# Kernel tuning notes

Measured on AMD Instinct MI355X. Metric: run time of the kernel, lower is better.

Reference implementation:

```python
import jax, jax.numpy as jnp
import numpy as np

D = 1024      # d_model
H = 16        # n_heads
HD = 64       # headdim
DFF = 2048    # per-expert ffn dim
E = 8         # n_experts
TOPK = 2
EPS = 1e-6
B, S = 2, 2048


def setup_inputs() -> dict:
    key = jax.random.key(0)
    ks = jax.random.split(key, 12)
    g = lambda i, shape, sc: (jax.random.normal(ks[i], shape, jnp.float32) * sc)
    return dict(
        x=g(0, (B, S, D), 1.0),
        pad_mask=jnp.ones((B, S), dtype=bool),
        norm1_w=jnp.ones((D,), jnp.float32),
        norm2_w=jnp.ones((D,), jnp.float32),
        Wr=g(1, (D, H * HD), 0.02),
        Wk=g(2, (D, H * HD), 0.02),
        Wv=g(3, (D, H * HD), 0.02),
        Wo=g(4, (H * HD, D), 0.02),
        decay=g(5, (H, HD), 0.5),   # time-decay param (w = exp(-exp(decay)))
        bonus=g(6, (H, HD), 0.5),   # RWKV 'u' first-token bonus
        router_w=g(7, (D, E), 0.02),
        w1=g(8, (E, D, DFF), 0.02),
        w2=g(9, (E, DFF, D), 0.02),
    )


def _rmsnorm(x, w):
    var = jnp.mean(x * x, axis=-1, keepdims=True)
    return x * jax.lax.rsqrt(var + EPS) * w


def _scan_dir(r, k, v, w, u):
    # r,k,v: [S,B,H,HD] ; w,u: [H,HD] ; RWKV-style linear-attention scan
    def step(St, rkv):
        r_t, k_t, v_t = rkv
        kv = jnp.einsum('bhk,bhv->bhkv', k_t, v_t)          # outer product
        y = jnp.einsum('bhk,bhkv->bhv', r_t, St + u[None, :, :, None] * kv)
        St = w[None, :, :, None] * St + kv                   # decayed state
        return St, y
    S0 = jnp.zeros((r.shape[1], H, HD, HD), r.dtype)
    _, ys = jax.lax.scan(step, S0, (r, k, v))
    return ys  # [S,B,H,HD]


def _bi_rwkv(x, pad_mask, Wr, Wk, Wv, Wo, decay, bonus):
    b, s, _ = x.shape
    r = (x @ Wr).reshape(b, s, H, HD)
    k = (x @ Wk).reshape(b, s, H, HD)
    v = (x @ Wv).reshape(b, s, H, HD)
    m = pad_mask[:, :, None, None].astype(x.dtype)
    k = k * m
    v = v * m
    w = jnp.exp(-jnp.exp(decay))  # decay in (0,1)
    rt = jnp.transpose(r, (1, 0, 2, 3))
    kt = jnp.transpose(k, (1, 0, 2, 3))
    vt = jnp.transpose(v, (1, 0, 2, 3))
    y_f = _scan_dir(rt, kt, vt, w, bonus)
    y_b = _scan_dir(rt[::-1], kt[::-1], vt[::-1], w, bonus)[::-1]
    y = jnp.transpose(y_f + y_b, (1, 0, 2, 3)).reshape(b, s, H * HD)
    return y @ Wo


def _moe_ffn(x, router_w, w1, w2):
    b, s, d = x.shape
    xt = x.reshape(-1, d)                                  # [T,D]
    T = xt.shape[0]
    probs = jax.nn.softmax(xt @ router_w, axis=-1)         # [T,E]
    topv, topi = jax.lax.top_k(probs, TOPK)
    gates = topv / jnp.sum(topv, axis=-1, keepdims=True)   # renormalized top-k
    gate_full = jnp.zeros((T, E), x.dtype).at[jnp.arange(T)[:, None], topi].set(gates)
    h = jax.nn.silu(jnp.einsum('td,edf->tef', xt, w1))     # all-expert dense ref
    out = jnp.einsum('tef,efd,te->td', h, w2, gate_full)
    # load-balancing aux loss
    frac = jnp.mean(jax.nn.one_hot(topi, E, dtype=x.dtype), axis=(0, 1))
    pmean = jnp.mean(probs, axis=0)
    aux = E * jnp.sum(frac * pmean)
    return out.reshape(b, s, d), aux


def reference(x, pad_mask, norm1_w, norm2_w, Wr, Wk, Wv, Wo, decay, bonus, router_w, w1, w2):
    # pre-norm RWKV block (dropout is identity at eval)
    x = x + _bi_rwkv(_rmsnorm(x, norm1_w), pad_mask, Wr, Wk, Wv, Wo, decay, bonus)
    ffn_out, aux = _moe_ffn(_rmsnorm(x, norm2_w), router_w, w1, w2)
    x = x + ffn_out
    return x, aux
```

## Files before the change

kernel.cpp:

```cpp
#include <hip/hip_runtime.h>

#define T_TOK 4096
#define DM 1024
#define NH 16
#define HDIM 64
#define DFF_ 2048
#define NE 8

typedef __bf16 bf16;
typedef __bf16 bf16x8 __attribute__((ext_vector_type(8)));
typedef __bf16 bf16x4 __attribute__((ext_vector_type(4)));
typedef float f32x4 __attribute__((ext_vector_type(4)));

__device__ __forceinline__ void gload_lds16(const bf16* g, bf16* l) {
  __builtin_amdgcn_global_load_lds(
      (const __attribute__((address_space(1))) void*)g,
      (__attribute__((address_space(3))) void*)l, 16, 0, 0);
}

template <int SPLIT>
__global__ __launch_bounds__(256) void rmsnorm_k(
    const float* __restrict__ x, const float* __restrict__ w,
    bf16* __restrict__ outh, bf16* __restrict__ outl) {
  const int t = blockIdx.x, tid = threadIdx.x;
  __shared__ float red[4];
  const f32x4 xv = *(const f32x4*)(x + (size_t)t * DM + tid * 4);
  float ss = xv.x * xv.x + xv.y * xv.y + xv.z * xv.z + xv.w * xv.w;
#pragma unroll
  for (int o = 32; o; o >>= 1) ss += __shfl_xor(ss, o);
  if ((tid & 63) == 0) red[tid >> 6] = ss;
  __syncthreads();
  const float rs = rsqrtf((red[0] + red[1] + red[2] + red[3]) * (1.f / DM) + 1e-6f);
  const f32x4 wv = *(const f32x4*)(w + tid * 4);
  float vv[4] = {xv.x * rs * wv.x, xv.y * rs * wv.y, xv.z * rs * wv.z, xv.w * rs * wv.w};
  bf16x4 h, l;
#pragma unroll
  for (int i = 0; i < 4; i++) {
    h[i] = (bf16)vv[i];
    l[i] = (bf16)(vv[i] - (float)h[i]);
  }
  *(bf16x4*)(outh + (size_t)t * DM + tid * 4) = h;
  if constexpr (SPLIT) *(bf16x4*)(outl + (size_t)t * DM + tid * 4) = l;
}

template <int SPLIT>
__global__ __launch_bounds__(256) void transpose_k(
    const float* __restrict__ src, bf16* __restrict__ dsth, bf16* __restrict__ dstl,
    int R, int C, long sstride, long dstride) {
  src += (long)blockIdx.z * sstride;
  dsth += (long)blockIdx.z * dstride;
  __shared__ float tle[32][33];
  const int tx = threadIdx.x, ty = threadIdx.y;
  const int c0 = blockIdx.x * 32, r0 = blockIdx.y * 32;
#pragma unroll
  for (int j = 0; j < 4; j++)
    tle[ty + 8 * j][tx] = src[(size_t)(r0 + ty + 8 * j) * C + c0 + tx];
  __syncthreads();
#pragma unroll
  for (int j = 0; j < 4; j++) {
    const float v = tle[tx][ty + 8 * j];
    const bf16 h = (bf16)v;
    dsth[(size_t)(c0 + ty + 8 * j) * R + r0 + tx] = h;
    if constexpr (SPLIT) {
      dstl[(size_t)(c0 + ty + 8 * j) * R + r0 + tx] = (bf16)(v - (float)h);
    }
  }
}

template <int K, int N, int MODE>
__global__ __launch_bounds__(256) void gemm_split_k(
    const bf16* __restrict__ Ah, const bf16* __restrict__ Al,
    const bf16* __restrict__ Bh, const bf16* __restrict__ Bl,
    float* __restrict__ Cout, const float* __restrict__ extraF,
    const int* __restrict__ pad) {
  __shared__ bf16 Ash[128 * 32], Asl[128 * 32], Bsh[128 * 32], Bsl[128 * 32];
  const int tid = threadIdx.x, w = tid >> 6, lane = tid & 63;
  const int n0 = blockIdx.x * 128, m0 = blockIdx.y * 128;
  const int sr0 = (w * 2 + 0) * 16 + (lane >> 2);
  const int sr1 = (w * 2 + 1) * 16 + (lane >> 2);
  const int sc = (lane & 3) * 8;
  const size_t ao0 = (size_t)(m0 + sr0) * K + sc, ao1 = (size_t)(m0 + sr1) * K + sc;
  const size_t bo0 = (size_t)(n0 + sr0) * K + sc, bo1 = (size_t)(n0 + sr1) * K + sc;

  f32x4 acc[4][4] = {};
  const int wm = w >> 1, wn = w & 1;
  const int fm = (wm * 64 + (lane & 15)) * 32 + (lane >> 4) * 8;
  const int fn = (wn * 64 + (lane & 15)) * 32 + (lane >> 4) * 8;
  const int l0 = (w * 2 + 0) * 512, l1 = (w * 2 + 1) * 512;

  for (int kt = 0; kt < K; kt += 32) {
    gload_lds16(Ah + ao0 + kt, Ash + l0);
    gload_lds16(Ah + ao1 + kt, Ash + l1);
    gload_lds16(Al + ao0 + kt, Asl + l0);
    gload_lds16(Al + ao1 + kt, Asl + l1);
    gload_lds16(Bh + bo0 + kt, Bsh + l0);
    gload_lds16(Bh + bo1 + kt, Bsh + l1);
    gload_lds16(Bl + bo0 + kt, Bsl + l0);
    gload_lds16(Bl + bo1 + kt, Bsl + l1);
    __syncthreads();
    bf16x8 afh[4], afl[4], bfh[4], bfl[4];
#pragma unroll
    for (int i = 0; i < 4; i++) {
      afh[i] = *(const bf16x8*)(Ash + fm + i * 512);
      afl[i] = *(const bf16x8*)(Asl + fm + i * 512);
      bfh[i] = *(const bf16x8*)(Bsh + fn + i * 512);
      bfl[i] = *(const bf16x8*)(Bsl + fn + i * 512);
    }
#pragma unroll
    for (int mi = 0; mi < 4; mi++)
#pragma unroll
      for (int ni = 0; ni < 4; ni++) {
        acc[mi][ni] = __builtin_amdgcn_mfma_f32_16x16x32_bf16(afh[mi], bfh[ni], acc[mi][ni], 0, 0, 0);
        acc[mi][ni] = __builtin_amdgcn_mfma_f32_16x16x32_bf16(afh[mi], bfl[ni], acc[mi][ni], 0, 0, 0);
        acc[mi][ni] = __builtin_amdgcn_mfma_f32_16x16x32_bf16(afl[mi], bfh[ni], acc[mi][ni], 0, 0, 0);
      }
    __syncthreads();
  }

  const int qr = (lane >> 4) * 4, cl = lane & 15;
#pragma unroll
  for (int mi = 0; mi < 4; mi++) {
#pragma unroll
    for (int r = 0; r < 4; r++) {
      const int row = m0 + wm * 64 + mi * 16 + qr + r;
      if constexpr (MODE == 0) {
        const float mf = (pad[row] != 0) ? 1.f : 0.f;
#pragma unroll
        for (int ni = 0; ni < 4; ni++) {
          const int col = n0 + wn * 64 + ni * 16 + cl;
          float v = acc[mi][ni][r];
          if (col >= DM) v *= mf;
          Cout[(size_t)row * N + col] = v;
        }
      } else {
#pragma unroll
        for (int ni = 0; ni < 4; ni++) {
          const int col = n0 + wn * 64 + ni * 16 + cl;
          Cout[(size_t)row * N + col] = acc[mi][ni][r] + extraF[(size_t)row * N + col];
        }
      }
    }
  }
}

template <int K, int MODE, int N>
__global__ __launch_bounds__(256) void gemm_k(
    const bf16* __restrict__ A, const bf16* __restrict__ BT, void* __restrict__ Cout,
    const float* __restrict__ extraF, const int* __restrict__ offsets,
    const int* __restrict__ counts, const int* __restrict__ ptoken) {
  __shared__ bf16 As[128 * 32];
  __shared__ bf16 Bs[128 * 32];
  const int tid = threadIdx.x, w = tid >> 6, lane = tid & 63;
  const int n0 = blockIdx.x * 128, m0 = blockIdx.y * 128;
  const int e = blockIdx.z;
  const int cnt = counts[e], offs = offsets[e];
  if (m0 >= cnt) return;
  const int sr0 = (w * 2 + 0) * 16 + (lane >> 2);
  const int sr1 = (w * 2 + 1) * 16 + (lane >> 2);
  const int sc = (lane & 3) * 8;
  const bf16 *a0, *a1;
  if constexpr (MODE == 2) {
    const int g0 = (m0 + sr0 < cnt) ? ptoken[offs + m0 + sr0] : 0;
    const int g1 = (m0 + sr1 < cnt) ? ptoken[offs + m0 + sr1] : 0;
    a0 = A + (size_t)g0 * K + sc;
    a1 = A + (size_t)g1 * K + sc;
  } else {
    const int g0 = offs + ((m0 + sr0 < cnt) ? m0 + sr0 : cnt - 1);
    const int g1 = offs + ((m0 + sr1 < cnt) ? m0 + sr1 : cnt - 1);
    a0 = A + (size_t)g0 * K + sc;
    a1 = A + (size_t)g1 * K + sc;
  }
  const bf16* btb = BT + (size_t)e * N * K;
  const bf16* b0 = btb + (size_t)(n0 + sr0) * K + sc;
  const bf16* b1 = btb + (size_t)(n0 + sr1) * K + sc;

  f32x4 acc[4][4] = {};
  const int wm = w >> 1, wn = w & 1;
  const int fm = (wm * 64 + (lane & 15)) * 32 + (lane >> 4) * 8;
  const int fn = (wn * 64 + (lane & 15)) * 32 + (lane >> 4) * 8;
  const int l0 = (w * 2 + 0) * 512, l1 = (w * 2 + 1) * 512;

  for (int kt = 0; kt < K; kt += 32) {
    gload_lds16(a0 + kt, As + l0);
    gload_lds16(a1 + kt, As + l1);
    gload_lds16(b0 + kt, Bs + l0);
    gload_lds16(b1 + kt, Bs + l1);
    __syncthreads();
    bf16x8 af[4], bfv[4];
#pragma unroll
    for (int i = 0; i < 4; i++) af[i] = *(const bf16x8*)(As + fm + i * 512);
#pragma unroll
    for (int i = 0; i < 4; i++) bfv[i] = *(const bf16x8*)(Bs + fn + i * 512);
#pragma unroll
    for (int mi = 0; mi < 4; mi++)
#pragma unroll
      for (int ni = 0; ni < 4; ni++)
        acc[mi][ni] =
            __builtin_amdgcn_mfma_f32_16x16x32_bf16(af[mi], bfv[ni], acc[mi][ni], 0, 0, 0);
    __syncthreads();
  }

  const int qr = (lane >> 4) * 4, cl = lane & 15;
#pragma unroll
  for (int mi = 0; mi < 4; mi++) {
#pragma unroll
    for (int r = 0; r < 4; r++) {
      const int row = m0 + wm * 64 + mi * 16 + qr + r;
      if (row >= cnt) continue;
      const size_t p = (size_t)(offs + row);
      if constexpr (MODE == 2) {
#pragma unroll
        for (int ni = 0; ni < 4; ni++) {
          const int col = n0 + wn * 64 + ni * 16 + cl;
          const float v = acc[mi][ni][r];
          ((bf16*)Cout)[p * N + col] = (bf16)(v / (1.f + __expf(-v)));
        }
      } else {
        const float g = extraF[p];
#pragma unroll
        for (int ni = 0; ni < 4; ni++) {
          const int col = n0 + wn * 64 + ni * 16 + cl;
          ((float*)Cout)[p * N + col] = acc[mi][ni][r] * g;
        }
      }
    }
  }
}

__global__ __launch_bounds__(256) void scan_k(
    const float* __restrict__ rkv, const float* __restrict__ decay,
    float* __restrict__ yacc) {
  const int wg = blockIdx.x;
  const int dir = wg & 1, kg = (wg >> 1) & 3, h = (wg >> 3) & 15, b = wg >> 7;
  const int tid = threadIdx.x, w = tid >> 6, lane = tid & 63;
  const int kb = kg * 16 + w * 4;
  __shared__ float ylds[4][16][64];

  const f32x4 dc = *(const f32x4*)(decay + h * HDIM + kb);
  const float wd0 = expf(-expf(dc.x)), wd1 = expf(-expf(dc.y));
  const float wd2 = expf(-expf(dc.z)), wd3 = expf(-expf(dc.w));

  const long base = (long)b * 2048 * 3072;
  const long start = dir ? (long)2047 * 3072 : 0;
  const long stp = dir ? -3072 : 3072;
  const float* rp = rkv + base + start + h * HDIM + kb;
  const float* kp = rp + 1024;
  const float* vp = rkv + base + start + 2048 + h * HDIM + lane;

  float S0 = 0.f, S1 = 0.f, S2 = 0.f, S3 = 0.f;
  f32x4 ka[8], ra[8], kc[8], rc[8];
  float va[8], vc[8], yb[16];
#pragma unroll
  for (int s = 0; s < 8; s++) {
    ka[s] = *(const f32x4*)(kp + (long)s * stp);
    ra[s] = *(const f32x4*)(rp + (long)s * stp);
    va[s] = vp[(long)s * stp];
  }
  for (int c = 0; c < 128; ++c) {
#pragma unroll
    for (int s = 0; s < 8; s++) {
      kc[s] = *(const f32x4*)(kp + (long)(8 + s) * stp);
      rc[s] = *(const f32x4*)(rp + (long)(8 + s) * stp);
      vc[s] = vp[(long)(8 + s) * stp];
    }
#pragma unroll
    for (int s = 0; s < 8; s++) {
      const float vv = va[s];
      const f32x4 Kv = ka[s], Rv = ra[s];
      yb[s] = Rv.x * S0 + Rv.y * S1 + Rv.z * S2 + Rv.w * S3;
      S0 = wd0 * S0 + Kv.x * vv;
      S1 = wd1 * S1 + Kv.y * vv;
      S2 = wd2 * S2 + Kv.z * vv;
      S3 = wd3 * S3 + Kv.w * vv;
    }
    if (c < 127) {
#pragma unroll
      for (int s = 0; s < 8; s++) {
        ka[s] = *(const f32x4*)(kp + (long)(16 + s) * stp);
        ra[s] = *(const f32x4*)(rp + (long)(16 + s) * stp);
        va[s] = vp[(long)(16 + s) * stp];
      }
    }
#pragma unroll
    for (int s = 0; s < 8; s++) {
      const float vv = vc[s];
      const f32x4 Kv = kc[s], Rv = rc[s];
      yb[8 + s] = Rv.x * S0 + Rv.y * S1 + Rv.z * S2 + Rv.w * S3;
      S0 = wd0 * S0 + Kv.x * vv;
      S1 = wd1 * S1 + Kv.y * vv;
      S2 = wd2 * S2 + Kv.z * vv;
      S3 = wd3 * S3 + Kv.w * vv;
    }
    kp += 16 * stp;
    rp += 16 * stp;
    vp += 16 * stp;
#pragma unroll
    for (int s = 0; s < 16; s++) ylds[w][s][lane] = yb[s];
    __syncthreads();
    {
      const int idx = tid * 4, tl = idx >> 6, v0 = idx & 63;
      const f32x4 s0 = *(const f32x4*)&ylds[0][tl][v0];
      const f32x4 s1 = *(const f32x4*)&ylds[1][tl][v0];
      const f32x4 s2 = *(const f32x4*)&ylds[2][tl][v0];
      const f32x4 s3 = *(const f32x4*)&ylds[3][tl][v0];
      const f32x4 sm = s0 + s1 + s2 + s3;
      const int sg = dir ? (2047 - (c * 16 + tl)) : (c * 16 + tl);
      float* yp = yacc + (size_t)(b * 2048 + sg) * DM + h * HDIM + v0;
      atomicAdd(yp + 0, sm.x);
      atomicAdd(yp + 1, sm.y);
      atomicAdd(yp + 2, sm.z);
      atomicAdd(yp + 3, sm.w);
    }
    __syncthreads();
  }
}

__global__ __launch_bounds__(256) void sum_k(
    const float* __restrict__ rkv, const float* __restrict__ bonus,
    const float* __restrict__ yacc, bf16* __restrict__ yh, bf16* __restrict__ yl) {
  const int tok = blockIdx.x, tid = threadIdx.x;
  const int hv = tid * 4;
  const float* bse = rkv + (size_t)tok * 3072;
  const f32x4 r4 = *(const f32x4*)(bse + hv);
  const f32x4 k4 = *(const f32x4*)(bse + 1024 + hv);
  const f32x4 v4 = *(const f32x4*)(bse + 2048 + hv);
  const f32x4 u4 = *(const f32x4*)(bonus + hv);
  float p = r4.x * u4.x * k4.x + r4.y * u4.y * k4.y + r4.z * u4.z * k4.z + r4.w * u4.w * k4.w;
  p += __shfl_xor(p, 1);
  p += __shfl_xor(p, 2);
  p += __shfl_xor(p, 4);
  p += __shfl_xor(p, 8);
  const float c2 = 2.f * p;
  const f32x4 ya = *(const f32x4*)(yacc + (size_t)tok * DM + hv);
  float yv[4] = {ya.x + c2 * v4.x, ya.y + c2 * v4.y, ya.z + c2 * v4.z, ya.w + c2 * v4.w};
  bf16x4 h, l;
#pragma unroll
  for (int i = 0; i < 4; i++) {
    h[i] = (bf16)yv[i];
    l[i] = (bf16)(yv[i] - (float)h[i]);
  }
  *(bf16x4*)(yh + (size_t)tok * DM + hv) = h;
  *(bf16x4*)(yl + (size_t)tok * DM + hv) = l;
}

__global__ __launch_bounds__(256) void router_k(
    const float* __restrict__ x2, const float* __restrict__ nw, const float* __restrict__ rw,
    float* __restrict__ gates, int* __restrict__ topi, float* __restrict__ prbuf) {
  const int t = blockIdx.x, tid = threadIdx.x, lane = tid & 63, wv = tid >> 6;
  __shared__ float red[4];
  __shared__ float lacc[4][8];
  const f32x4 xv = *(const f32x4*)(x2 + (size_t)t * DM + tid * 4);
  float ss = xv.x * xv.x + xv.y * xv.y + xv.z * xv.z + xv.w * xv.w;
#pragma unroll
  for (int o = 32; o; o >>= 1) ss += __shfl_xor(ss, o);
  if (!lane) red[wv] = ss;
  __syncthreads();
  const float rs = rsqrtf((red[0] + red[1] + red[2] + red[3]) * (1.f / DM) + 1e-6f);
  const f32x4 wv4 = *(const f32x4*)(nw + tid * 4);
  float a[8] = {0, 0, 0, 0, 0, 0, 0, 0};
  const float xns[4] = {xv.x * rs * wv4.x, xv.y * rs * wv4.y, xv.z * rs * wv4.z,
                        xv.w * rs * wv4.w};
#pragma unroll
  for (int j = 0; j < 4; j++) {
    const float* rwp = rw + (size_t)(tid * 4 + j) * NE;
    const f32x4 q0 = *(const f32x4*)rwp;
    const f32x4 q1 = *(const f32x4*)(rwp + 4);
    a[0] += xns[j] * q0.x; a[1] += xns[j] * q0.y; a[2] += xns[j] * q0.z; a[3] += xns[j] * q0.w;
    a[4] += xns[j] * q1.x; a[5] += xns[j] * q1.y; a[6] += xns[j] * q1.z; a[7] += xns[j] * q1.w;
  }
#pragma unroll
  for (int e2 = 0; e2 < 8; e2++) {
    float v = a[e2];
#pragma unroll
    for (int o = 32; o; o >>= 1) v += __shfl_xor(v, o);
    a[e2] = v;
  }
  if (!lane) {
#pragma unroll
    for (int e2 = 0; e2 < 8; e2++) lacc[wv][e2] = a[e2];
  }
  __syncthreads();
  if (tid == 0) {
    float l[8];
    for (int e2 = 0; e2 < 8; e2++)
      l[e2] = lacc[0][e2] + lacc[1][e2] + lacc[2][e2] + lacc[3][e2];
    float mx = l[0];
    for (int e2 = 1; e2 < 8; e2++) mx = fmaxf(mx, l[e2]);
    float pr[8], s = 0.f;
    for (int e2 = 0; e2 < 8; e2++) { pr[e2] = expf(l[e2] - mx); s += pr[e2]; }
    const float inv = 1.f / s;
    for (int e2 = 0; e2 < 8; e2++) pr[e2] *= inv;
    int i1 = 0; float v1 = pr[0];
    for (int e2 = 1; e2 < 8; e2++) if (pr[e2] > v1) { v1 = pr[e2]; i1 = e2; }
    int i2 = -1; float v2 = -1.f;
    for (int e2 = 0; e2 < 8; e2++) if (e2 != i1 && pr[e2] > v2) { v2 = pr[e2]; i2 = e2; }
    const float dn = 1.f / (v1 + v2);
    gates[t * 2] = v1 * dn;
    gates[t * 2 + 1] = v2 * dn;
    topi[t * 2] = i1;
    topi[t * 2 + 1] = i2;
    f32x4 p0, p1;
    p0.x = pr[0]; p0.y = pr[1]; p0.z = pr[2]; p0.w = pr[3];
    p1.x = pr[4]; p1.y = pr[5]; p1.z = pr[6]; p1.w = pr[7];
    *(f32x4*)(prbuf + t * 8) = p0;
    *(f32x4*)(prbuf + t * 8 + 4) = p1;
  }
}

__global__ __launch_bounds__(256) void route_k(
    const int* __restrict__ topi, const float* __restrict__ gates,
    const float* __restrict__ prbuf,
    int* __restrict__ offsets, int* __restrict__ counts,
    int* __restrict__ ptoken, float* __restrict__ pgate, int* __restrict__ ppos,
    float* __restrict__ auxout) {
  const int tid = threadIdx.x;
  __shared__ int hist[256][8];
  __shared__ float pshr[256][8];
  __shared__ int pfx[256][8];
  __shared__ int chunksum[8][8], chunkbase[8][8];
  __shared__ float chunkp[8][8];
  __shared__ int ctot[8], offs_s[8];
  __shared__ float ptot[8];

  int lh[8] = {0, 0, 0, 0, 0, 0, 0, 0};
#pragma unroll 4
  for (int j = 0; j < 32; j++) lh[topi[tid * 32 + j]]++;
  float ps[8] = {0, 0, 0, 0, 0, 0, 0, 0};
  for (int j = 0; j < 16; j++) {
    const int tok = tid * 16 + j;
    const f32x4 q0 = *(const f32x4*)(prbuf + tok * 8);
    const f32x4 q1 = *(const f32x4*)(prbuf + tok * 8 + 4);
    ps[0] += q0.x; ps[1] += q0.y; ps[2] += q0.z; ps[3] += q0.w;
    ps[4] += q1.x; ps[5] += q1.y; ps[6] += q1.z; ps[7] += q1.w;
  }
#pragma unroll
  for (int e = 0; e < 8; e++) { hist[tid][e] = lh[e]; pshr[tid][e] = ps[e]; }
  __syncthreads();
  if (tid < 64) {
    const int e = tid >> 3, c = tid & 7;
    int s = 0;
    float p = 0.f;
    for (int t2 = c * 32; t2 < c * 32 + 32; t2++) { s += hist[t2][e]; p += pshr[t2][e]; }
    chunksum[c][e] = s;
    chunkp[c][e] = p;
  }
  __syncthreads();
  if (tid < 8) {
    int run = 0;
    float pr = 0.f;
    for (int c = 0; c < 8; c++) {
      chunkbase[c][tid] = run;
      run += chunksum[c][tid];
      pr += chunkp[c][tid];
    }
    ctot[tid] = run;
    ptot[tid] = pr;
  }
  __syncthreads();
  if (tid == 0) {
    int o = 0;
    float a = 0.f;
    for (int e = 0; e < 8; e++) {
      offs_s[e] = o;
      offsets[e] = o;
      counts[e] = ctot[e];
      a += (float)ctot[e] * ptot[e];
      o += ctot[e];
    }
    auxout[0] = a * (8.f / (8192.f * 4096.f));
  }
  if (tid < 64) {
    const int e = tid >> 3, c = tid & 7;
    int run = 0;
    for (int t2 = c * 32; t2 < c * 32 + 32; t2++) {
      pfx[t2][e] = run;
      run += hist[t2][e];
    }
  }
  __syncthreads();
  int rc[8] = {0, 0, 0, 0, 0, 0, 0, 0};
  const int cb = tid >> 5;
#pragma unroll 4
  for (int j = 0; j < 32; j++) {
    const int slot = tid * 32 + j;
    const int e = topi[slot];
    const int pos = offs_s[e] + chunkbase[cb][e] + pfx[tid][e] + rc[e]++;
    ptoken[pos] = slot >> 1;
    pgate[pos] = gates[slot];
    ppos[slot] = pos;
  }
}

__global__ __launch_bounds__(256) void final_k(
    const float* __restrict__ x2, const float* __restrict__ pout,
    const int* __restrict__ ppos, float* __restrict__ out) {
  const int idx = blockIdx.x * 256 + threadIdx.x;
  const int t = idx >> 8, c = (idx & 255) * 4;
  const int p0 = ppos[t * 2], p1 = ppos[t * 2 + 1];
  const f32x4 a = *(const f32x4*)(x2 + (size_t)t * DM + c);
  const f32x4 b0 = *(const f32x4*)(pout + (size_t)p0 * DM + c);
  const f32x4 b1 = *(const f32x4*)(pout + (size_t)p1 * DM + c);
  const f32x4 o = a + b0 + b1;
  *(f32x4*)(out + (size_t)t * DM + c) = o;
}

extern "C" void kernel_launch(void* const* d_in, const int* in_sizes, int n_in,
                              void* d_out, int out_size, void* d_ws, size_t ws_size,
                              hipStream_t stream) {
  (void)in_sizes; (void)n_in; (void)out_size; (void)ws_size;
  const float* x = (const float*)d_in[0];
  const int* pad = (const int*)d_in[1];
  const float* n1w = (const float*)d_in[2];
  const float* n2w = (const float*)d_in[3];
  const float* Wr = (const float*)d_in[4];
  const float* Wk = (const float*)d_in[5];
  const float* Wv = (const float*)d_in[6];
  const float* Wo = (const float*)d_in[7];
  const float* decay = (const float*)d_in[8];
  const float* bonus = (const float*)d_in[9];
  const float* rw = (const float*)d_in[10];
  const float* w1 = (const float*)d_in[11];
  const float* w2 = (const float*)d_in[12];
  float* out = (float*)d_out;
  char* ws = (char*)d_ws;

  float* rkv = (float*)(ws + 0);
  float* yacc = (float*)(ws + 50331648);
  float* x2 = (float*)(ws + 67108864);
  bf16* xh = (bf16*)(ws + 83886080);
  bf16* xl = (bf16*)(ws + 92274688);
  bf16* wbh = (bf16*)(ws + 100663296);
  bf16* wbl = (bf16*)(ws + 106954752);
  float* pout = (float*)(ws + 113246208);
  bf16* hbuf = (bf16*)(ws + 146800640);
  char* sm = ws + 180355072;
  int* counts = (int*)(sm);
  int* offsets = (int*)(sm + 64);
  int* topi = (int*)(sm + 128);
  float* gates = (float*)(sm + 32896);
  int* ppos = (int*)(sm + 65664);
  int* ptoken = (int*)(sm + 98432);
  float* pgate = (float*)(sm + 131712);
  float* prbuf = (float*)(sm + 164480);
  bf16* w1t = (bf16*)(ws + 0);
  bf16* w2t = (bf16*)(ws + 33554432);
  bf16* woh = wbh;
  bf16* wol = (bf16*)(ws + 102760448);

  const dim3 tb(32, 8);

  rmsnorm_k<1><<<4096, 256, 0, stream>>>(x, n1w, xh, xl);
  transpose_k<1><<<dim3(32, 32, 1), tb, 0, stream>>>(Wr, wbh, wbl, 1024, 1024, 0, 0);
  transpose_k<1><<<dim3(32, 32, 1), tb, 0, stream>>>(Wk, wbh + 1048576, wbl + 1048576, 1024, 1024, 0, 0);
  transpose_k<1><<<dim3(32, 32, 1), tb, 0, stream>>>(Wv, wbh + 2097152, wbl + 2097152, 1024, 1024, 0, 0);
  gemm_split_k<1024, 3072, 0><<<dim3(24, 32, 1), 256, 0, stream>>>(
      xh, xl, wbh, wbl, rkv, nullptr, pad);
  hipMemsetAsync(yacc, 0, 16777216, stream);
  scan_k<<<256, 256, 0, stream>>>(rkv, decay, yacc);
  transpose_k<1><<<dim3(32, 32, 1), tb, 0, stream>>>(Wo, woh, wol, 1024, 1024, 0, 0);
  sum_k<<<4096, 256, 0, stream>>>(rkv, bonus, yacc, xh, xl);
  gemm_split_k<1024, 1024, 1><<<dim3(8, 32, 1), 256, 0, stream>>>(
      xh, xl, woh, wol, x2, x, nullptr);
  rmsnorm_k<0><<<4096, 256, 0, stream>>>(x2, n2w, xh, nullptr);
  router_k<<<4096, 256, 0, stream>>>(x2, n2w, rw, gates, topi, prbuf);
  route_k<<<1, 256, 0, stream>>>(topi, gates, prbuf, offsets, counts, ptoken, pgate,
                                 ppos, out + 4194304);
  transpose_k<0><<<dim3(64, 32, 8), tb, 0, stream>>>(
      w1, w1t, nullptr, 1024, 2048, (long)1024 * 2048, (long)1024 * 2048);
  transpose_k<0><<<dim3(32, 64, 8), tb, 0, stream>>>(
      w2, w2t, nullptr, 2048, 1024, (long)2048 * 1024, (long)2048 * 1024);
  gemm_k<1024, 2, 2048><<<dim3(16, 64, 8), 256, 0, stream>>>(
      xh, w1t, hbuf, nullptr, offsets, counts, ptoken);
  gemm_k<2048, 3, 1024><<<dim3(8, 64, 8), 256, 0, stream>>>(
      hbuf, w2t, pout, pgate, offsets, counts, nullptr);
  final_k<<<4096, 256, 0, stream>>>(x2, pout, ppos, out);
}
```

Measured before the change: 977.4 us.

## Replace scan atomics with per-split partial buffers and widen per-thread state

The bidirectional RWKV scan now gives each thread 8 key dimensions instead of 4, which halves the grid to 128 workgroups and raises per-step instruction-level parallelism. Instead of atomically adding into a zeroed accumulator, each (direction, key-half) split writes its own partial output plane with plain vector stores. The memset goes away, and sum_k reduces the four partial planes. This removes global atomic contention and the memset, at the cost of more register pressure, fewer workgroups for the GPU's many compute units, and extra read traffic in sum_k.

```diff
diff --git a/kernel.cpp b/kernel.cpp
--- a/kernel.cpp
+++ b/kernel.cpp
@@ -227,18 +227,18 @@
   }
 }
 
-__global__ __launch_bounds__(256) void scan_k(
+__global__ __launch_bounds__(256, 1) void scan_k(
     const float* __restrict__ rkv, const float* __restrict__ decay,
-    float* __restrict__ yacc) {
+    float* __restrict__ ypf) {
   const int wg = blockIdx.x;
-  const int dir = wg & 1, kg = (wg >> 1) & 3, h = (wg >> 3) & 15, b = wg >> 7;
+  const int dir = wg & 1, kg2 = (wg >> 1) & 1, h = (wg >> 2) & 15, b = wg >> 6;
   const int tid = threadIdx.x, w = tid >> 6, lane = tid & 63;
-  const int kb = kg * 16 + w * 4;
+  const int kb = kg2 * 32 + w * 8;
   __shared__ float ylds[4][16][64];
 
-  const f32x4 dc = *(const f32x4*)(decay + h * HDIM + kb);
-  const float wd0 = expf(-expf(dc.x)), wd1 = expf(-expf(dc.y));
-  const float wd2 = expf(-expf(dc.z)), wd3 = expf(-expf(dc.w));
+  float wd[8];
+#pragma unroll
+  for (int i = 0; i < 8; i++) wd[i] = expf(-expf(decay[h * HDIM + kb + i]));
 
   const long base = (long)b * 2048 * 3072;
   const long start = dir ? (long)2047 * 3072 : 0;
@@ -247,55 +247,40 @@
   const float* kp = rp + 1024;
   const float* vp = rkv + base + start + 2048 + h * HDIM + lane;
 
-  float S0 = 0.f, S1 = 0.f, S2 = 0.f, S3 = 0.f;
-  f32x4 ka[8], ra[8], kc[8], rc[8];
-  float va[8], vc[8], yb[16];
-#pragma unroll
-  for (int s = 0; s < 8; s++) {
-    ka[s] = *(const f32x4*)(kp + (long)s * stp);
-    ra[s] = *(const f32x4*)(rp + (long)s * stp);
-    va[s] = vp[(long)s * stp];
-  }
+  float S[8];
+#pragma unroll
+  for (int i = 0; i < 8; i++) S[i] = 0.f;
+
+  float rA[8][8], kA[8][8], vA[8], rB[8][8], kB[8][8], vB[8];
+
+#define LOADH(RB, KB, VB, NT)                                              \
+  _Pragma("unroll") for (int s = 0; s < 8; s++) {                          \
+    *(f32x4*)&RB[s][0] = *(const f32x4*)(rp + (long)((NT) + s) * stp);     \
+    *(f32x4*)&RB[s][4] = *(const f32x4*)(rp + (long)((NT) + s) * stp + 4); \
+    *(f32x4*)&KB[s][0] = *(const f32x4*)(kp + (long)((NT) + s) * stp);     \
+    *(f32x4*)&KB[s][4] = *(const f32x4*)(kp + (long)((NT) + s) * stp + 4); \
+    VB[s] = vp[(long)((NT) + s) * stp];                                    \
+  }
+#define COMPH(RB, KB, VB, QOFF)                                            \
+  _Pragma("unroll") for (int s = 0; s < 8; s++) {                          \
+    const float vv = VB[s];                                                \
+    float y = 0.f;                                                         \
+    _Pragma("unroll") for (int i = 0; i < 8; i++) {                        \
+      y += RB[s][i] * S[i];                                                \
+      S[i] = wd[i] * S[i] + KB[s][i] * vv;                                 \
+    }                                                                      \
+    ylds[w][(QOFF) + s][lane] = y;                                         \
+  }
+
+  LOADH(rA, kA, vA, 0);
   for (int c = 0; c < 128; ++c) {
-#pragma unroll
-    for (int s = 0; s < 8; s++) {
-      kc[s] = *(const f32x4*)(kp + (long)(8 + s) * stp);
-      rc[s] = *(const f32x4*)(rp + (long)(8 + s) * stp);
-      vc[s] = vp[(long)(8 + s) * stp];
-    }
-#pragma unroll
-    for (int s = 0; s < 8; s++) {
-      const float vv = va[s];
-      const f32x4 Kv = ka[s], Rv = ra[s];
-      yb[s] = Rv.x * S0 + Rv.y * S1 + Rv.z * S2 + Rv.w * S3;
-      S0 = wd0 * S0 + Kv.x * vv;
-      S1 = wd1 * S1 + Kv.y * vv;
-      S2 = wd2 * S2 + Kv.z * vv;
-      S3 = wd3 * S3 + Kv.w * vv;
-    }
-    if (c < 127) {
-#pragma unroll
-      for (int s = 0; s < 8; s++) {
-        ka[s] = *(const f32x4*)(kp + (long)(16 + s) * stp);
-        ra[s] = *(const f32x4*)(rp + (long)(16 + s) * stp);
-        va[s] = vp[(long)(16 + s) * stp];
-      }
-    }
-#pragma unroll
-    for (int s = 0; s < 8; s++) {
-      const float vv = vc[s];
-      const f32x4 Kv = kc[s], Rv = rc[s];
-      yb[8 + s] = Rv.x * S0 + Rv.y * S1 + Rv.z * S2 + Rv.w * S3;
-      S0 = wd0 * S0 + Kv.x * vv;
-      S1 = wd1 * S1 + Kv.y * vv;
-      S2 = wd2 * S2 + Kv.z * vv;
-      S3 = wd3 * S3 + Kv.w * vv;
-    }
+    LOADH(rB, kB, vB, 8);
+    COMPH(rA, kA, vA, 0);
+    if (c < 127) { LOADH(rA, kA, vA, 16); }
+    COMPH(rB, kB, vB, 8);
+    rp += 16 * stp;
     kp += 16 * stp;
-    rp += 16 * stp;
     vp += 16 * stp;
-#pragma unroll
-    for (int s = 0; s < 16; s++) ylds[w][s][lane] = yb[s];
     __syncthreads();
     {
       const int idx = tid * 4, tl = idx >> 6, v0 = idx & 63;
@@ -305,19 +290,18 @@
       const f32x4 s3 = *(const f32x4*)&ylds[3][tl][v0];
       const f32x4 sm = s0 + s1 + s2 + s3;
       const int sg = dir ? (2047 - (c * 16 + tl)) : (c * 16 + tl);
-      float* yp = yacc + (size_t)(b * 2048 + sg) * DM + h * HDIM + v0;
-      atomicAdd(yp + 0, sm.x);
-      atomicAdd(yp + 1, sm.y);
-      atomicAdd(yp + 2, sm.z);
-      atomicAdd(yp + 3, sm.w);
+      *(f32x4*)(ypf + ((size_t)(dir * 2 + kg2) * T_TOK + (b * 2048 + sg)) * DM +
+                h * HDIM + v0) = sm;
     }
     __syncthreads();
   }
+#undef LOADH
+#undef COMPH
 }
 
 __global__ __launch_bounds__(256) void sum_k(
     const float* __restrict__ rkv, const float* __restrict__ bonus,
-    const float* __restrict__ yacc, bf16* __restrict__ yh, bf16* __restrict__ yl) {
+    const float* __restrict__ ypf, bf16* __restrict__ yh, bf16* __restrict__ yl) {
   const int tok = blockIdx.x, tid = threadIdx.x;
   const int hv = tid * 4;
   const float* bse = rkv + (size_t)tok * 3072;
@@ -331,13 +315,19 @@
   p += __shfl_xor(p, 4);
   p += __shfl_xor(p, 8);
   const float c2 = 2.f * p;
-  const f32x4 ya = *(const f32x4*)(yacc + (size_t)tok * DM + hv);
-  float yv[4] = {ya.x + c2 * v4.x, ya.y + c2 * v4.y, ya.z + c2 * v4.z, ya.w + c2 * v4.w};
+  f32x4 acc;
+  acc.x = c2 * v4.x; acc.y = c2 * v4.y; acc.z = c2 * v4.z; acc.w = c2 * v4.w;
+#pragma unroll
+  for (int st = 0; st < 4; ++st) {
+    const f32x4 yv = *(const f32x4*)(ypf + ((size_t)st * T_TOK + tok) * DM + hv);
+    acc.x += yv.x; acc.y += yv.y; acc.z += yv.z; acc.w += yv.w;
+  }
+  float yv4[4] = {acc.x, acc.y, acc.z, acc.w};
   bf16x4 h, l;
 #pragma unroll
   for (int i = 0; i < 4; i++) {
-    h[i] = (bf16)yv[i];
-    l[i] = (bf16)(yv[i] - (float)h[i]);
+    h[i] = (bf16)yv4[i];
+    l[i] = (bf16)(yv4[i] - (float)h[i]);
   }
   *(bf16x4*)(yh + (size_t)tok * DM + hv) = h;
   *(bf16x4*)(yl + (size_t)tok * DM + hv) = l;
@@ -525,12 +515,12 @@
   char* ws = (char*)d_ws;
 
   float* rkv = (float*)(ws + 0);
-  float* yacc = (float*)(ws + 50331648);
   float* x2 = (float*)(ws + 67108864);
   bf16* xh = (bf16*)(ws + 83886080);
   bf16* xl = (bf16*)(ws + 92274688);
   bf16* wbh = (bf16*)(ws + 100663296);
   bf16* wbl = (bf16*)(ws + 106954752);
+  float* ypf = (float*)(ws + 113246208);
   float* pout = (float*)(ws + 113246208);
   bf16* hbuf = (bf16*)(ws + 146800640);
   char* sm = ws + 180355072;
@@ -555,10 +545,9 @@
   transpose_k<1><<<dim3(32, 32, 1), tb, 0, stream>>>(Wv, wbh + 2097152, wbl + 2097152, 1024, 1024, 0, 0);
   gemm_split_k<1024, 3072, 0><<<dim3(24, 32, 1), 256, 0, stream>>>(
       xh, xl, wbh, wbl, rkv, nullptr, pad);
-  hipMemsetAsync(yacc, 0, 16777216, stream);
-  scan_k<<<256, 256, 0, stream>>>(rkv, decay, yacc);
+  scan_k<<<128, 256, 0, stream>>>(rkv, decay, ypf);
   transpose_k<1><<<dim3(32, 32, 1), tb, 0, stream>>>(Wo, woh, wol, 1024, 1024, 0, 0);
-  sum_k<<<4096, 256, 0, stream>>>(rkv, bonus, yacc, xh, xl);
+  sum_k<<<4096, 256, 0, stream>>>(rkv, bonus, ypf, xh, xl);
   gemm_split_k<1024, 1024, 1><<<dim3(8, 32, 1), 256, 0, stream>>>(
       xh, xl, woh, wol, x2, x, nullptr);
   rmsnorm_k<0><<<4096, 256, 0, stream>>>(x2, n2w, xh, nullptr);
```

Result: faster. 847.5 us (-13.3%).
